# Optimization experiments

Measured on AMD Instinct MI355X. Metric: run time of the kernel, lower is better.

Reference implementation:

```python
import jax, jax.numpy as jnp
import numpy as np

K = 3
STRIDE = 1
PAD = 1

def conv2d(x, w, b, stride, padding):
    out = jax.lax.conv_general_dilated(x, w, (stride, stride), [(padding, padding), (padding, padding)],
                                       dimension_numbers=('NCHW', 'OIHW', 'NCHW'))
    if b is not None:
        out = out + b[None, :, None, None]
    return out

def deform_conv2d(x, offset, mask, weight, stride, padding):
    # torchvision-style modulated deformable conv (offset_groups=1, groups=1)
    B, C, H, W = x.shape
    C2 = weight.shape[0]
    KK = K * K
    Hout, Wout = offset.shape[2], offset.shape[3]
    off = offset.reshape(B, KK, 2, Hout, Wout)  # (dy, dx) pairs per kernel tap
    ky = jnp.repeat(jnp.arange(K), K)  # kernel row per tap [KK]
    kx = jnp.tile(jnp.arange(K), K)    # kernel col per tap [KK]
    base_y = (jnp.arange(Hout) * stride - padding).astype(jnp.float32)
    base_x = (jnp.arange(Wout) * stride - padding).astype(jnp.float32)
    py = off[:, :, 0] + ky[None, :, None, None] + base_y[None, None, :, None]  # [B,KK,Hout,Wout]
    px = off[:, :, 1] + kx[None, :, None, None] + base_x[None, None, None, :]
    y0f = jnp.floor(py); x0f = jnp.floor(px)
    ly = py - y0f; lx = px - x0f
    y0 = y0f.astype(jnp.int32); x0 = x0f.astype(jnp.int32)
    xf = x.reshape(B, C, H * W)

    def corner(yi, xi, wgt):
        valid = (yi >= 0) & (yi < H) & (xi >= 0) & (xi < W)
        idx = (jnp.clip(yi, 0, H - 1) * W + jnp.clip(xi, 0, W - 1)).reshape(B, -1)  # [B, KK*Hout*Wout]
        v = jax.vmap(lambda xb, ib: xb[:, ib])(xf, idx)  # [B, C, KK*Hout*Wout]
        return v * (wgt * valid).reshape(B, 1, -1)

    val = (corner(y0, x0, (1.0 - ly) * (1.0 - lx))
           + corner(y0, x0 + 1, (1.0 - ly) * lx)
           + corner(y0 + 1, x0, ly * (1.0 - lx))
           + corner(y0 + 1, x0 + 1, ly * lx))
    val = val * mask.reshape(B, 1, -1)  # modulation per (tap, spatial)
    val = val.reshape(B, C, KK, Hout, Wout)
    out = jnp.einsum('bckhw,ock->bohw', val, weight.reshape(C2, C, KK))
    return out

def setup_inputs() -> dict:
    key = jax.random.key(0)
    ks = jax.random.split(key, 6)
    B, C1, C2, H, W = 8, 256, 256, 64, 64
    x = jax.random.normal(ks[0], (B, C1, H, W), jnp.float32)
    offset_w = jax.random.normal(ks[1], (2 * K * K, C1, K, K), jnp.float32) * 0.01
    offset_b = jax.random.normal(ks[2], (2 * K * K,), jnp.float32) * 0.5
    mod_w = jax.random.normal(ks[3], (K * K, C1, K, K), jnp.float32) * 0.01
    mod_b = jnp.zeros((K * K,), jnp.float32)
    reg_w = jax.random.normal(ks[4], (C2, C1, K, K), jnp.float32) * np.float32(1.0 / np.sqrt(C1 * K * K))
    return {"x": x, "offset_w": offset_w, "offset_b": offset_b, "mod_w": mod_w, "mod_b": mod_b, "reg_w": reg_w}

def reference(x, offset_w, offset_b, mod_w, mod_b, reg_w):
    h, w = x.shape[2], x.shape[3]
    max_offset = max(h, w) / 4.0
    offset = jnp.clip(conv2d(x, offset_w, offset_b, STRIDE, PAD), -max_offset, max_offset)
    modulator = jax.nn.sigmoid(conv2d(x, mod_w, mod_b, STRIDE, PAD))
    return deform_conv2d(x, offset, modulator, reg_w, STRIDE, PAD)
```

## Files before the change

kernel.cpp:

```cpp
#include <hip/hip_runtime.h>
#include <math.h>

#define BB 8
#define CIN 256
#define COUT 256
#define HH 64
#define WW 64
#define OCM 27
#define KTOT 2304
#define NKT 72

typedef unsigned int u32;
typedef unsigned short u16;

#define WS_XBF 0
#define WS_W2 16777216
#define WS_W2OM 17956864
#define WS_OFFMOD 18104320

__device__ __forceinline__ u16 f2bf(float f) {
    u32 u = __float_as_uint(f);
    u32 r = (u + 0x7FFFu + ((u >> 16) & 1u)) >> 16;
    return (u16)r;
}

typedef __attribute__((address_space(1))) const unsigned int* gptr_t;
typedef __attribute__((address_space(3))) unsigned int* lptr_t;
__device__ __forceinline__ void gl2lds16(const void* g, void* l) {
    __builtin_amdgcn_global_load_lds((gptr_t)g, (lptr_t)l, 16, 0, 0);
}

typedef __attribute__((ext_vector_type(8))) short frag;
typedef __attribute__((ext_vector_type(4))) float f4;

__device__ __forceinline__ int sw_off(int row, int oct) {
    return (row << 5) + ((oct ^ (row & 3)) << 3);
}

#define BARRIER_RAW() do { asm volatile("" ::: "memory"); \
    __builtin_amdgcn_s_barrier(); asm volatile("" ::: "memory"); } while (0)

__global__ __launch_bounds__(256) void k_nhwc2(const float* __restrict__ x,
                                               u16* __restrict__ xbf) {
    const int y = blockIdx.x, b = blockIdx.y;
    __shared__ float T[64][65];
    const int wl = threadIdx.x & 63, g = threadIdx.x >> 6;
    for (int c0 = 0; c0 < 256; c0 += 64) {
#pragma unroll
        for (int i = 0; i < 16; ++i) {
            int c = g + i * 4;
            T[c][wl] = x[(((size_t)(b * 256 + c0 + c)) << 12) + (y << 6) + wl];
        }
        __syncthreads();
#pragma unroll
        for (int j = 0; j < 16; ++j) {
            int w = g * 16 + j;
            xbf[((((size_t)b << 12) + (y << 6) + w) << 8) + c0 + wl] = f2bf(T[wl][w]);
        }
        __syncthreads();
    }
}

__global__ void k_pack_w2(const float* __restrict__ rw, u16* __restrict__ w2) {
    int o = blockIdx.x * blockDim.x + threadIdx.x;
    if (o >= NKT * COUT * 32) return;
    int kk = o & 31;
    int n = (o >> 5) & 255;
    int kt = o >> 13;
    int k = kt * 32 + kk;
    int tap = k >> 8;
    int c = k & 255;
    w2[o] = f2bf(rw[n * KTOT + c * 9 + tap]);
}

__global__ void k_pack_w2om(const float* __restrict__ ow, const float* __restrict__ mw,
                            u16* __restrict__ w2om) {
    int o = blockIdx.x * blockDim.x + threadIdx.x;
    if (o >= NKT * 32 * 32) return;
    int kk = o & 31;
    int oc = (o >> 5) & 31;
    int kt = o >> 10;
    int k = kt * 32 + kk;
    int tap = k >> 8;
    int c = k & 255;
    float v = 0.f;
    if (oc < 18) v = ow[oc * KTOT + c * 9 + tap];
    else if (oc < 27) v = mw[(oc - 18) * KTOT + c * 9 + tap];
    w2om[o] = f2bf(v);
}

__global__ __launch_bounds__(512, 4) void k_offmod5(
    const u16* __restrict__ xbf, const u16* __restrict__ w2om,
    const float* __restrict__ ob, const float* __restrict__ mb,
    float* __restrict__ offmod)
{
    const int h = blockIdx.x, b = blockIdx.y;
    const int t = threadIdx.x;
    const int lane = t & 63, wv = t >> 6;
    const int hf = wv >> 2;
    const int wl4 = wv & 3;
    const int th = t & 255;
    const int fr = lane & 15, q = lane >> 4;
    const int wm = wl4 << 4;
    const int mg = th >> 2, oct = th & 3;

    __shared__ u16 AsB[2][2][64 * 32];
    __shared__ u16 BsB[2][2][32 * 32];
    __shared__ float red[64][33];

    const u16* xb = xbf + ((size_t)b << 20);
    const int kbase = hf * 36;

    auto loadA = [&](int kt, uint4* r) {
        int tap = kt >> 3;
        int yy = h + tap / 3 - 1, xx = mg + tap % 3 - 1;
        int c0 = ((kt & 7) << 5) + (oct << 3);
        uint4 v = make_uint4(0, 0, 0, 0);
        if ((unsigned)yy < HH && (unsigned)xx < WW)
            v = *(const uint4*)(xb + (((size_t)yy << 6) + xx) * 256 + c0);
        *r = v;
    };
    auto loadB = [&](int kt, uint4* r) {
        if (th < 128) *r = *(const uint4*)(w2om + (size_t)kt * 1024 + (th >> 2) * 32 + (th & 3) * 8);
    };
    auto storeAB = [&](int buf, uint4* rA, uint4* rB) {
        *(uint4*)&AsB[hf][buf][sw_off(mg, oct)] = *rA;
        if (th < 128) *(uint4*)&BsB[hf][buf][sw_off(th >> 2, th & 3)] = *rB;
    };

    f4 acc[2];
    acc[0] = (f4){0.f, 0.f, 0.f, 0.f};
    acc[1] = (f4){0.f, 0.f, 0.f, 0.f};

    uint4 rA0, rB0, rA1, rB1;
    loadA(kbase, &rA0); loadB(kbase, &rB0);
    storeAB(0, &rA0, &rB0);
    loadA(kbase + 1, &rA1); loadB(kbase + 1, &rB1);
    asm volatile("s_waitcnt lgkmcnt(0)" ::: "memory");

    auto body = [&](int i, int p, uint4* cA, uint4* cB, uint4* nA, uint4* nB) {
        BARRIER_RAW();
        frag a  = *(const frag*)&AsB[hf][p][sw_off(wm + fr, q)];
        frag b0 = *(const frag*)&BsB[hf][p][sw_off(fr, q)];
        frag b1 = *(const frag*)&BsB[hf][p][sw_off(16 + fr, q)];
        if (i + 2 < 36) { loadA(kbase + i + 2, nA); loadB(kbase + i + 2, nB); }
        if (i + 1 < 36) storeAB(1 - p, cA, cB);
        acc[0] = __builtin_amdgcn_mfma_f32_16x16x32_bf16(a, b0, acc[0], 0, 0, 0);
        acc[1] = __builtin_amdgcn_mfma_f32_16x16x32_bf16(a, b1, acc[1], 0, 0, 0);
        asm volatile("s_waitcnt lgkmcnt(0)" ::: "memory");
    };
    for (int i = 0; i < 36; i += 2) {
        body(i, 0, &rA1, &rB1, &rA0, &rB0);
        body(i + 1, 1, &rA0, &rB0, &rA1, &rB1);
    }

    if (hf == 1) {
#pragma unroll
        for (int ni = 0; ni < 2; ++ni)
#pragma unroll
            for (int r = 0; r < 4; ++r)
                red[wm + q * 4 + r][ni * 16 + fr] = acc[ni][r];
    }
    __syncthreads();
    if (hf == 0) {
#pragma unroll
        for (int ni = 0; ni < 2; ++ni) {
            int oc = ni * 16 + fr;
            if (oc >= OCM) continue;
            bool is_off = oc < 18;
            float bias = is_off ? ob[oc] : mb[oc - 18];
            float4 v;
            float* vp = (float*)&v;
#pragma unroll
            for (int r = 0; r < 4; ++r) {
                float s = acc[ni][r] + red[wm + q * 4 + r][oc] + bias;
                vp[r] = is_off ? fminf(fmaxf(s, -16.f), 16.f)
                               : 1.f / (1.f + __expf(-s));
            }
            *(float4*)&offmod[(((size_t)b * OCM + oc) << 12) + (h << 6) + wm + q * 4] = v;
        }
    }
}

__global__ __launch_bounds__(512, 4) void k_deform6(
    const u16* __restrict__ xbf, const float* __restrict__ offmod,
    const u16* __restrict__ w2, float* __restrict__ out)
{
    const int t = threadIdx.x;
    const int h = blockIdx.x, b = blockIdx.y;
    const int lane = t & 63, wv = t >> 6;

    __shared__ int   SIDX[9][4][64];
    __shared__ float SW[9][4][64];
    __shared__ u16 AsB[2][64 * 32];
    __shared__ u16 BsB[2][256 * 32];

    const float* om = offmod + (size_t)b * OCM * 4096;
    for (int e = t; e < 9 * 64; e += 512) {
        int m = e & 63, tap = e >> 6;
        float dy = om[(tap * 2) * 4096 + h * 64 + m];
        float dx = om[(tap * 2 + 1) * 4096 + h * 64 + m];
        float mv = om[(18 + tap) * 4096 + h * 64 + m];
        float py = dy + (float)(tap / 3) + (float)(h - 1);
        float px = dx + (float)(tap % 3) + (float)(m - 1);
        float y0f = floorf(py), x0f = floorf(px);
        float ly = py - y0f, lx = px - x0f;
        int y0 = (int)y0f, x0 = (int)x0f;
        int   ysr[2] = {y0, y0 + 1};
        int   xsr[2] = {x0, x0 + 1};
        float wy[2] = {1.f - ly, ly};
        float wx[2] = {1.f - lx, lx};
#pragma unroll
        for (int r = 0; r < 4; ++r) {
            int yy = ysr[r >> 1], xx = xsr[r & 1];
            bool ok = ((unsigned)yy < HH) && ((unsigned)xx < WW);
            int yc = min(max(yy, 0), HH - 1);
            int xc = min(max(xx, 0), WW - 1);
            SIDX[tap][r][m] = yc * WW + xc;
            SW[tap][r][m] = ok ? (wy[r >> 1] * wx[r & 1] * mv) : 0.f;
        }
    }
    __syncthreads();

    if (wv < 4) {
        const int fr = lane & 15, q = lane >> 4;
        const int wn = wv << 6;

        f4 acc[4][4];
#pragma unroll
        for (int mi = 0; mi < 4; ++mi)
#pragma unroll
            for (int ni = 0; ni < 4; ++ni) acc[mi][ni] = (f4){0.f, 0.f, 0.f, 0.f};

        for (int kt = 0; kt < NKT; ++kt) {
            const int p = kt & 1;
            BARRIER_RAW();
            frag a[4];
#pragma unroll
            for (int mi = 0; mi < 4; ++mi)
                a[mi] = *(const frag*)&AsB[p][sw_off(mi * 16 + fr, q)];
#pragma unroll
            for (int nh = 0; nh < 2; ++nh) {
                frag b0 = *(const frag*)&BsB[p][sw_off(wn + nh * 32 + fr, q)];
                frag b1 = *(const frag*)&BsB[p][sw_off(wn + nh * 32 + 16 + fr, q)];
#pragma unroll
                for (int mi = 0; mi < 4; ++mi) {
                    acc[mi][nh * 2]     = __builtin_amdgcn_mfma_f32_16x16x32_bf16(
                        a[mi], b0, acc[mi][nh * 2], 0, 0, 0);
                    acc[mi][nh * 2 + 1] = __builtin_amdgcn_mfma_f32_16x16x32_bf16(
                        a[mi], b1, acc[mi][nh * 2 + 1], 0, 0, 0);
                }
            }
        }

#pragma unroll
        for (int ni = 0; ni < 4; ++ni) {
            int n_g = wn + ni * 16 + fr;
            float* outn = out + (((size_t)b * COUT + n_g) << 12) + (h << 6);
#pragma unroll
            for (int mi = 0; mi < 4; ++mi) {
                int wl = mi * 16 + q * 4;
                *(float4*)&outn[wl] = make_float4(acc[mi][ni][0], acc[mi][ni][1],
                                                  acc[mi][ni][2], acc[mi][ni][3]);
            }
        }
    } else {
        const int pt = t - 256;
        const int mg = pt >> 2, oct = pt & 3;
        const int pwv = wv - 4;
        const int ko_sw = (lane & 3) ^ ((lane >> 2) & 3);
        const u16* xpl = xbf + ((size_t)b << 20);

        auto stageB = [&](int kt, int buf) {
            const u16* src = w2 + ((size_t)kt << 13);
#pragma unroll
            for (int j = 0; j < 4; ++j) {
                int n = (pwv << 6) + (j << 4) + (lane >> 2);
                u16* dst = &BsB[buf][((pwv << 6) + (j << 4)) << 5];
                gl2lds16(src + n * 32 + ko_sw * 8, dst);
            }
        };
        auto loadCorners = [&](int kt, uint4 (&cr)[4]) {
            int tap = kt >> 3;
            int c0 = ((kt & 7) << 5) + (oct << 3);
            const u16* base = xpl + c0;
#pragma unroll
            for (int r = 0; r < 4; ++r)
                cr[r] = *(const uint4*)(base + ((size_t)SIDX[tap][r][mg] << 8));
        };
        auto interpStore = [&](int kt, int buf, uint4 (&cr)[4]) {
            int tap = kt >> 3;
            float va[8];
#pragma unroll
            for (int j = 0; j < 8; ++j) va[j] = 0.f;
#pragma unroll
            for (int r = 0; r < 4; ++r) {
                float s = SW[tap][r][mg];
                u32 uu[4] = {cr[r].x, cr[r].y, cr[r].z, cr[r].w};
#pragma unroll
                for (int jj = 0; jj < 4; ++jj) {
                    va[2 * jj]     += s * __uint_as_float(uu[jj] << 16);
                    va[2 * jj + 1] += s * __uint_as_float(uu[jj] & 0xFFFF0000u);
                }
            }
            u32 pk[4];
#pragma unroll
            for (int jp = 0; jp < 4; ++jp)
                pk[jp] = (u32)f2bf(va[2 * jp]) | ((u32)f2bf(va[2 * jp + 1]) << 16);
            *(uint4*)&AsB[buf][sw_off(mg, oct)] = make_uint4(pk[0], pk[1], pk[2], pk[3]);
        };

        uint4 crA[4], crB[4];
        stageB(0, 0);
        loadCorners(0, crB);
        loadCorners(1, crA);
        interpStore(0, 0, crB);
        asm volatile("s_waitcnt lgkmcnt(0)" ::: "memory");

        auto pstep = [&](int kt, int p, uint4 (&cur)[4], uint4 (&nxt)[4]) {
            if (kt == NKT - 1) asm volatile("s_waitcnt vmcnt(0)" ::: "memory");
            else               asm volatile("s_waitcnt vmcnt(4)" ::: "memory");
            BARRIER_RAW();
            if (kt + 1 < NKT) stageB(kt + 1, 1 - p);
            if (kt + 2 < NKT) loadCorners(kt + 2, nxt);
            if (kt + 1 < NKT) interpStore(kt + 1, 1 - p, cur);
            asm volatile("s_waitcnt lgkmcnt(0)" ::: "memory");
        };
        for (int kt = 0; kt < NKT; kt += 2) {
            pstep(kt, 0, crA, crB);
            pstep(kt + 1, 1, crB, crA);
        }
    }
}

extern "C" void kernel_launch(void* const* d_in, const int* in_sizes, int n_in,
                              void* d_out, int out_size, void* d_ws, size_t ws_size,
                              hipStream_t stream) {
    const float* x  = (const float*)d_in[0];
    const float* ow = (const float*)d_in[1];
    const float* ob = (const float*)d_in[2];
    const float* mw = (const float*)d_in[3];
    const float* mb = (const float*)d_in[4];
    const float* rw = (const float*)d_in[5];
    float* out = (float*)d_out;
    char* ws = (char*)d_ws;

    u16*   xbf    = (u16*)(ws + WS_XBF);
    u16*   w2     = (u16*)(ws + WS_W2);
    u16*   w2om   = (u16*)(ws + WS_W2OM);
    float* offmod = (float*)(ws + WS_OFFMOD);

    k_nhwc2<<<dim3(HH, BB), 256, 0, stream>>>(x, xbf);
    k_pack_w2<<<(NKT * COUT * 32 + 255) / 256, 256, 0, stream>>>(rw, w2);
    k_pack_w2om<<<(NKT * 32 * 32 + 255) / 256, 256, 0, stream>>>(ow, mw, w2om);
    k_offmod5<<<dim3(HH, BB), 512, 0, stream>>>(xbf, w2om, ob, mb, offmod);
    k_deform6<<<dim3(HH, BB), 512, 0, stream>>>(xbf, offmod, w2, out);
}
```

Before: 204.7 us.

## Deepen corner prefetch, retune LDS swizzle, pack transpose stores, interleave block order

The deform kernel's producer waves now prefetch bilinear corner samples three K-tiles ahead instead of two, rotating across three register buffers, to hide gather latency. The LDS swizzle for the A tile and the B staging lane swizzle change to use bits 1-2 of the row, aiming to cut bank conflicts. The NHWC transpose writes two packed bf16 values per 32-bit store, and the offmod/deform grids become 1D with batch in the low bits so neighbouring blocks share weights and rows in cache. The extra prefetch buffer raises register pressure, and the swizzle change has to match how the MFMA side reads the tile.

```diff
diff --git a/kernel.cpp b/kernel.cpp
--- a/kernel.cpp
+++ b/kernel.cpp
@@ -34,17 +34,20 @@
 typedef __attribute__((ext_vector_type(4))) float f4;
 
 __device__ __forceinline__ int sw_off(int row, int oct) {
-    return (row << 5) + ((oct ^ (row & 3)) << 3);
+    return (row << 5) + ((oct ^ ((row >> 1) & 3)) << 3);
 }
 
 #define BARRIER_RAW() do { asm volatile("" ::: "memory"); \
     __builtin_amdgcn_s_barrier(); asm volatile("" ::: "memory"); } while (0)
 
-__global__ __launch_bounds__(256) void k_nhwc2(const float* __restrict__ x,
+__global__ __launch_bounds__(256) void k_nhwc3(const float* __restrict__ x,
                                                u16* __restrict__ xbf) {
     const int y = blockIdx.x, b = blockIdx.y;
     __shared__ float T[64][65];
-    const int wl = threadIdx.x & 63, g = threadIdx.x >> 6;
+    const int t = threadIdx.x;
+    const int wl = t & 63, g = t >> 6;
+    const int pr = wl & 31, wsub = wl >> 5;
+    u32* xo = (u32*)xbf;
     for (int c0 = 0; c0 < 256; c0 += 64) {
 #pragma unroll
         for (int i = 0; i < 16; ++i) {
@@ -53,9 +56,10 @@
         }
         __syncthreads();
 #pragma unroll
-        for (int j = 0; j < 16; ++j) {
-            int w = g * 16 + j;
-            xbf[((((size_t)b << 12) + (y << 6) + w) << 8) + c0 + wl] = f2bf(T[wl][w]);
+        for (int j = 0; j < 8; ++j) {
+            int w = j * 8 + g * 2 + wsub;
+            u32 v = (u32)f2bf(T[2 * pr][w]) | ((u32)f2bf(T[2 * pr + 1][w]) << 16);
+            xo[((((size_t)b << 12) + (y << 6) + w) << 7) + (c0 >> 1) + pr] = v;
         }
         __syncthreads();
     }
@@ -89,12 +93,12 @@
     w2om[o] = f2bf(v);
 }
 
-__global__ __launch_bounds__(512, 4) void k_offmod5(
+__global__ __launch_bounds__(512, 4) void k_offmod6(
     const u16* __restrict__ xbf, const u16* __restrict__ w2om,
     const float* __restrict__ ob, const float* __restrict__ mb,
     float* __restrict__ offmod)
 {
-    const int h = blockIdx.x, b = blockIdx.y;
+    const int b = blockIdx.x & 7, h = blockIdx.x >> 3;
     const int t = threadIdx.x;
     const int lane = t & 63, wv = t >> 6;
     const int hf = wv >> 2;
@@ -182,12 +186,12 @@
     }
 }
 
-__global__ __launch_bounds__(512, 4) void k_deform6(
+__global__ __launch_bounds__(512, 4) void k_deform7(
     const u16* __restrict__ xbf, const float* __restrict__ offmod,
     const u16* __restrict__ w2, float* __restrict__ out)
 {
     const int t = threadIdx.x;
-    const int h = blockIdx.x, b = blockIdx.y;
+    const int b = blockIdx.x & 7, h = blockIdx.x >> 3;
     const int lane = t & 63, wv = t >> 6;
 
     __shared__ int   SIDX[9][4][64];
@@ -268,7 +272,7 @@
         const int pt = t - 256;
         const int mg = pt >> 2, oct = pt & 3;
         const int pwv = wv - 4;
-        const int ko_sw = (lane & 3) ^ ((lane >> 2) & 3);
+        const int ko_sw = (lane & 3) ^ ((lane >> 3) & 3);
         const u16* xpl = xbf + ((size_t)b << 20);
 
         auto stageB = [&](int kt, int buf) {
@@ -310,25 +314,30 @@
             *(uint4*)&AsB[buf][sw_off(mg, oct)] = make_uint4(pk[0], pk[1], pk[2], pk[3]);
         };
 
-        uint4 crA[4], crB[4];
+        uint4 cr0[4], cr1[4], cr2[4];
         stageB(0, 0);
-        loadCorners(0, crB);
-        loadCorners(1, crA);
-        interpStore(0, 0, crB);
+        loadCorners(0, cr0);
+        loadCorners(1, cr1);
+        loadCorners(2, cr2);
+        interpStore(0, 0, cr0);
         asm volatile("s_waitcnt lgkmcnt(0)" ::: "memory");
 
         auto pstep = [&](int kt, int p, uint4 (&cur)[4], uint4 (&nxt)[4]) {
-            if (kt == NKT - 1) asm volatile("s_waitcnt vmcnt(0)" ::: "memory");
-            else               asm volatile("s_waitcnt vmcnt(4)" ::: "memory");
+            if (kt + 2 < NKT) asm volatile("s_waitcnt vmcnt(4)" ::: "memory");
+            else              asm volatile("s_waitcnt vmcnt(0)" ::: "memory");
             BARRIER_RAW();
             if (kt + 1 < NKT) stageB(kt + 1, 1 - p);
-            if (kt + 2 < NKT) loadCorners(kt + 2, nxt);
+            if (kt + 3 < NKT) loadCorners(kt + 3, nxt);
             if (kt + 1 < NKT) interpStore(kt + 1, 1 - p, cur);
             asm volatile("s_waitcnt lgkmcnt(0)" ::: "memory");
         };
-        for (int kt = 0; kt < NKT; kt += 2) {
-            pstep(kt, 0, crA, crB);
-            pstep(kt + 1, 1, crB, crA);
+        for (int kt = 0; kt < NKT; kt += 6) {
+            pstep(kt,     0, cr1, cr0);
+            pstep(kt + 1, 1, cr2, cr1);
+            pstep(kt + 2, 0, cr0, cr2);
+            pstep(kt + 3, 1, cr1, cr0);
+            pstep(kt + 4, 0, cr2, cr1);
+            pstep(kt + 5, 1, cr0, cr2);
         }
     }
 }
@@ -350,9 +359,9 @@
     u16*   w2om   = (u16*)(ws + WS_W2OM);
     float* offmod = (float*)(ws + WS_OFFMOD);
 
-    k_nhwc2<<<dim3(HH, BB), 256, 0, stream>>>(x, xbf);
+    k_nhwc3<<<dim3(HH, BB), 256, 0, stream>>>(x, xbf);
     k_pack_w2<<<(NKT * COUT * 32 + 255) / 256, 256, 0, stream>>>(rw, w2);
     k_pack_w2om<<<(NKT * 32 * 32 + 255) / 256, 256, 0, stream>>>(ow, mw, w2om);
-    k_offmod5<<<dim3(HH, BB), 512, 0, stream>>>(xbf, w2om, ob, mb, offmod);
-    k_deform6<<<dim3(HH, BB), 512, 0, stream>>>(xbf, offmod, w2, out);
-}
+    k_offmod6<<<dim3(512), 512, 0, stream>>>(xbf, w2om, ob, mb, offmod);
+    k_deform7<<<dim3(512), 512, 0, stream>>>(xbf, offmod, w2, out);
+}
```

After: 182.8 us. 1.12x faster.
